# Kernel tuning notes

Hardware: AMD Instinct MI355X
Metric: run time of the kernel (lower is better)

Reference implementation:

```python
import jax, jax.numpy as jnp
import numpy as np

B, C, T, H, W = 4, 256, 16, 16, 16
C2 = C // 2  # 128


def setup_inputs() -> dict:
    key = jax.random.key(0)
    ks = jax.random.split(key, 12)
    s = 1.0 / np.sqrt(C)
    return {
        "X": jax.random.normal(ks[0], (B, C, T, H, W), dtype=jnp.float32),
        "pe": jax.random.uniform(ks[1], (C, T, H, W), dtype=jnp.float32),
        "task_q": jax.random.uniform(ks[2], (C2, T, H, W), dtype=jnp.float32),
        "task_k": jax.random.uniform(ks[3], (C2, T, H, W), dtype=jnp.float32),
        "task_v": jax.random.uniform(ks[4], (C2, T, H, W), dtype=jnp.float32),
        "Wq": jax.random.normal(ks[5], (C2, C), dtype=jnp.float32) * s,
        "bq": jnp.zeros((C2,), dtype=jnp.float32),
        "Wk": jax.random.normal(ks[6], (C2, C), dtype=jnp.float32) * s,
        "bk": jnp.zeros((C2,), dtype=jnp.float32),
        "Wv": jax.random.normal(ks[7], (C2, C), dtype=jnp.float32) * s,
        "bv": jnp.zeros((C2,), dtype=jnp.float32),
        "Wo": jax.random.normal(ks[8], (C, C2), dtype=jnp.float32) * s,
    }


def reference(X, pe, task_q, task_k, task_v, Wq, bq, Wk, bk, Wv, bv, Wo):
    b, c, t, h, w = X.shape
    c2 = Wq.shape[0]
    n = t * h * w
    Xp = X + pe  # broadcast [C,T,H,W] over batch

    def proj(Wm, bm, task):
        # 1x1x1 Conv3d == channel contraction; add bias and per-task offset
        y = jnp.einsum('bcthw,oc->bothw', Xp, Wm)
        return y + bm[:, None, None, None] + task  # [B,C2,T,H,W]

    q = proj(Wq, bq, task_q).reshape(b, c2, n).transpose(0, 2, 1)  # [B,N,C2]
    k = proj(Wk, bk, task_k).reshape(b, c2, n)                     # [B,C2,N]
    sim = jnp.matmul(q, k)                                         # [B,N,N]
    v = proj(Wv, bv, task_v).reshape(b, c2, n).transpose(0, 2, 1)  # [B,N,C2]
    # NOTE: original torch code computes softmax(sim) but then multiplies by
    # the RAW similarity matrix (softmax output is dead code). Faithful math:
    out = jnp.matmul(sim, v)                                       # [B,N,C2]
    # torch .reshape of contiguous [B,N,C2] -> [B,C2,T,H,W] (layout reinterpret)
    out = out.reshape(b, c2, t, h, w)
    out = jnp.einsum('bcthw,oc->bothw', out, Wo)  # out_conv, no bias
    return out + X
```

## Files before the change

kernel.cpp:

```cpp
#include <hip/hip_runtime.h>
#include <cstddef>

#define BB 4
#define CCH 256
#define C2 128
#define NN 4096
#define PM 384
#define KVS 32

typedef __attribute__((ext_vector_type(8))) short short8v;
typedef __attribute__((ext_vector_type(4))) short short4v;
typedef __attribute__((ext_vector_type(4))) float f32x4;

static __device__ __forceinline__ short f2bf(float f) {
    union { float f; unsigned u; } c; c.f = f;
    unsigned r = (c.u + 0x7FFFu + ((c.u >> 16) & 1u)) >> 16;
    return (short)r;
}

__global__ __launch_bounds__(256) void k_pack(
    const float* __restrict__ Wq, const float* __restrict__ bq,
    const float* __restrict__ Wk, const float* __restrict__ bk,
    const float* __restrict__ Wv, const float* __restrict__ bv,
    const float* __restrict__ Wo,
    short* __restrict__ wpackh, float* __restrict__ bpack,
    short* __restrict__ Woh)
{
    const int m = blockIdx.x;
    const int c = threadIdx.x;
    if (m < PM) {
        const float* w; const float* bs; int mm;
        if (m < C2)        { w = Wq; bs = bq; mm = m; }
        else if (m < 2*C2) { w = Wk; bs = bk; mm = m - C2; }
        else               { w = Wv; bs = bv; mm = m - 2*C2; }
        wpackh[m * CCH + c] = f2bf(w[mm * CCH + c]);
        if (c == 0) bpack[m] = bs[mm];
    } else {
        const int o = m - PM;
        if (c < C2) Woh[o * C2 + c] = f2bf(Wo[o * C2 + c]);
    }
}

__global__ __launch_bounds__(256) void k_xph(
    const float* __restrict__ X, const float* __restrict__ pe,
    short* __restrict__ XpH)
{
    const size_t e8 = ((size_t)blockIdx.x * 256 + threadIdx.x) * 8;
    const size_t r  = e8 & (size_t)(CCH * NN - 1);
    float4 x0 = *(const float4*)&X[e8];
    float4 x1 = *(const float4*)&X[e8 + 4];
    float4 p0 = *(const float4*)&pe[r];
    float4 p1 = *(const float4*)&pe[r + 4];
    short8v o;
    o[0] = f2bf(x0.x + p0.x); o[1] = f2bf(x0.y + p0.y);
    o[2] = f2bf(x0.z + p0.z); o[3] = f2bf(x0.w + p0.w);
    o[4] = f2bf(x1.x + p1.x); o[5] = f2bf(x1.y + p1.y);
    o[6] = f2bf(x1.z + p1.z); o[7] = f2bf(x1.w + p1.w);
    *(short8v*)&XpH[e8] = o;
}

#define LROW 40
#define TSP  136
__global__ __launch_bounds__(256) void k_projm(
    const short* __restrict__ XpH,
    const float* __restrict__ tq, const float* __restrict__ tk,
    const float* __restrict__ tv,
    const short* __restrict__ wpackh, const float* __restrict__ bpack,
    short* __restrict__ qt, short* __restrict__ kk, short* __restrict__ vv)
{
    __shared__ short smem[17408];
    short* As = smem;
    short* Bs = smem + 5120;
    const int b  = blockIdx.z;
    const int m0 = blockIdx.y * 128;
    const int n0 = blockIdx.x * 128;
    const int tid  = threadIdx.x;
    const int wave = tid >> 6;
    const int lane = tid & 63;
    const int lr = lane & 15, lg = lane >> 4;
    const int wm = wave >> 1, wn = wave & 1;
    const short* __restrict__ Xb = XpH + (size_t)b * CCH * NN;

    const int am  = tid >> 1;
    const int akb = tid & 1;
    const int cq  = tid >> 5;
    const int nq  = tid & 31;

    f32x4 acc[4][4];
#pragma unroll
    for (int i = 0; i < 4; ++i)
#pragma unroll
        for (int j = 0; j < 4; ++j) acc[i][j] = (f32x4){0.f, 0.f, 0.f, 0.f};

    for (int k0 = 0; k0 < CCH; k0 += 32) {
        {
            const size_t gsrc = (size_t)(m0 + am) * CCH + k0 + akb * 16;
            *(short8v*)&As[am * LROW + akb * 16]     = *(const short8v*)&wpackh[gsrc];
            *(short8v*)&As[am * LROW + akb * 16 + 8] = *(const short8v*)&wpackh[gsrc + 8];
        }
        short sreg[4][4];
#pragma unroll
        for (int j = 0; j < 4; ++j) {
            const int c = k0 + cq * 4 + j;
            short4v xv = *(const short4v*)&Xb[(size_t)c * NN + n0 + nq * 4];
            sreg[j][0] = xv.x; sreg[j][1] = xv.y; sreg[j][2] = xv.z; sreg[j][3] = xv.w;
        }
#pragma unroll
        for (int i = 0; i < 4; ++i) {
            short4v v; v.x = sreg[0][i]; v.y = sreg[1][i]; v.z = sreg[2][i]; v.w = sreg[3][i];
            *(short4v*)&Bs[(nq * 4 + i) * LROW + cq * 4] = v;
        }
        __syncthreads();
        short8v a[4], bfr[4];
#pragma unroll
        for (int fm = 0; fm < 4; ++fm)
            a[fm] = *(const short8v*)&As[(wm * 64 + fm * 16 + lr) * LROW + lg * 8];
#pragma unroll
        for (int fn = 0; fn < 4; ++fn)
            bfr[fn] = *(const short8v*)&Bs[(wn * 64 + fn * 16 + lr) * LROW + lg * 8];
#pragma unroll
        for (int fm = 0; fm < 4; ++fm)
#pragma unroll
            for (int fn = 0; fn < 4; ++fn)
                acc[fm][fn] = __builtin_amdgcn_mfma_f32_16x16x32_bf16(
                    a[fm], bfr[fn], acc[fm][fn], 0, 0, 0);
        __syncthreads();
    }

    short* Ts = smem;
    const int sel = m0 >> 7;
    if (sel == 0) {
#pragma unroll
        for (int fm = 0; fm < 4; ++fm)
#pragma unroll
            for (int fn = 0; fn < 4; ++fn) {
                const int n_l  = wn * 64 + fn * 16 + lr;
                const int m_lb = wm * 64 + fm * 16 + lg * 4;
                short4v v;
#pragma unroll
                for (int r = 0; r < 4; ++r) {
                    const int m_l = m_lb + r;
                    v[r] = f2bf(acc[fm][fn][r] + bpack[m_l]
                                + tq[(size_t)m_l * NN + n0 + n_l]);
                }
                *(short4v*)&Ts[n_l * TSP + m_lb] = v;
            }
        __syncthreads();
        const int n_l = tid >> 1, half = tid & 1;
        short* dst = qt + (size_t)b * NN * C2 + (size_t)(n0 + n_l) * C2 + half * 64;
        const short* src = &Ts[n_l * TSP + half * 64];
#pragma unroll
        for (int q2 = 0; q2 < 8; ++q2)
            *(short8v*)&dst[q2 * 8] = *(const short8v*)&src[q2 * 8];
    } else {
        const float* __restrict__ task = (sel == 1) ? tk : tv;
        short* kv = (sel == 1) ? kk : vv;
#pragma unroll
        for (int fm = 0; fm < 4; ++fm)
#pragma unroll
            for (int fn = 0; fn < 4; ++fn) {
                const int n_l = wn * 64 + fn * 16 + lr;
#pragma unroll
                for (int r = 0; r < 4; ++r) {
                    const int m_l = wm * 64 + fm * 16 + lg * 4 + r;
                    Ts[m_l * TSP + n_l] =
                        f2bf(acc[fm][fn][r] + bpack[m0 + m_l]
                             + task[(size_t)m_l * NN + n0 + n_l]);
                }
            }
        __syncthreads();
        const int m_l = tid >> 1, half = tid & 1;
        short* dst = kv + (size_t)b * C2 * NN + (size_t)m_l * NN + n0 + half * 64;
        const short* src = &Ts[m_l * TSP + half * 64];
#pragma unroll
        for (int q2 = 0; q2 < 8; ++q2)
            *(short8v*)&dst[q2 * 8] = *(const short8v*)&src[q2 * 8];
    }
}

__global__ __launch_bounds__(256) void k_kv(
    const short* __restrict__ kk, const short* __restrict__ vv,
    float* __restrict__ Mpart)
{
    const int b = blockIdx.y, s = blockIdx.x;
    const int tid = threadIdx.x;
    const int wave = tid >> 6, lane = tid & 63;
    const int lr = lane & 15, lg = lane >> 4;
    const int wi = wave >> 1, wj = wave & 1;
    const short* Kb = kk + (size_t)b * C2 * NN;
    const short* Vb = vv + (size_t)b * C2 * NN;
    const int nbase = s * 128;
    f32x4 acc[4][4];
#pragma unroll
    for (int i = 0; i < 4; ++i)
#pragma unroll
        for (int j = 0; j < 4; ++j) acc[i][j] = (f32x4){0.f, 0.f, 0.f, 0.f};

    for (int ks = 0; ks < 4; ++ks) {
        const int nn = nbase + ks * 32 + lg * 8;
        short8v a[4], bv8[4];
#pragma unroll
        for (int fi = 0; fi < 4; ++fi)
            a[fi] = *(const short8v*)&Kb[(size_t)(wi * 64 + fi * 16 + lr) * NN + nn];
#pragma unroll
        for (int fj = 0; fj < 4; ++fj)
            bv8[fj] = *(const short8v*)&Vb[(size_t)(wj * 64 + fj * 16 + lr) * NN + nn];
#pragma unroll
        for (int fi = 0; fi < 4; ++fi)
#pragma unroll
            for (int fj = 0; fj < 4; ++fj)
                acc[fi][fj] = __builtin_amdgcn_mfma_f32_16x16x32_bf16(
                    a[fi], bv8[fj], acc[fi][fj], 0, 0, 0);
    }
    float* Mp = Mpart + ((size_t)b * KVS + s) * C2 * C2;
#pragma unroll
    for (int fi = 0; fi < 4; ++fi)
#pragma unroll
        for (int fj = 0; fj < 4; ++fj) {
            const int j = wj * 64 + fj * 16 + lr;
#pragma unroll
            for (int r = 0; r < 4; ++r) {
                const int i = wi * 64 + fi * 16 + lg * 4 + r;
                Mp[(size_t)i * C2 + j] = acc[fi][fj][r];
            }
        }
}

__global__ __launch_bounds__(256) void k_kvred(
    const float* __restrict__ Mpart, short* __restrict__ Mt)
{
    const int b = blockIdx.y;
    const int i = blockIdx.x * 16 + (threadIdx.x >> 4);
    const int j0 = (threadIdx.x & 15) * 8;
    const float* p = Mpart + (size_t)b * KVS * C2 * C2 + (size_t)i * C2 + j0;
    float a8[8];
#pragma unroll
    for (int e = 0; e < 8; ++e) a8[e] = 0.f;
    for (int s = 0; s < KVS; ++s) {
        float4 v0 = *(const float4*)&p[(size_t)s * C2 * C2];
        float4 v1 = *(const float4*)&p[(size_t)s * C2 * C2 + 4];
        a8[0] += v0.x; a8[1] += v0.y; a8[2] += v0.z; a8[3] += v0.w;
        a8[4] += v1.x; a8[5] += v1.y; a8[6] += v1.z; a8[7] += v1.w;
    }
    short* mt = Mt + (size_t)b * C2 * C2;
#pragma unroll
    for (int e = 0; e < 8; ++e)
        mt[(size_t)(j0 + e) * C2 + i] = f2bf(a8[e]);
}

#define PSP 136
__global__ __launch_bounds__(256) void k_qmfinal(
    const short* __restrict__ qt, const short* __restrict__ Mt,
    const short* __restrict__ Woh,
    const float* __restrict__ X, float* __restrict__ out)
{
    __shared__ short Ps[64 * PSP];
    const int g  = blockIdx.x;
    const int jh = blockIdx.y;
    const int b  = blockIdx.z;
    const int tid = threadIdx.x;
    const int wave = tid >> 6, lane = tid & 63;
    const int lr = lane & 15, lg = lane >> 4;
    const short* Qb = qt + (size_t)b * NN * C2;
    const short* Mb = Mt + (size_t)b * C2 * C2;

    {
        const int wc = wave >> 1, wj = wave & 1;
        f32x4 acc1[4][2];
#pragma unroll
        for (int i = 0; i < 4; ++i)
#pragma unroll
            for (int j = 0; j < 2; ++j) acc1[i][j] = (f32x4){0.f, 0.f, 0.f, 0.f};
        for (int ks = 0; ks < 4; ++ks) {
            const int kb = ks * 32 + lg * 8;
            short8v a1[4], b1[2];
#pragma unroll
            for (int fc = 0; fc < 4; ++fc) {
                const int c = wc * 64 + fc * 16 + lr;
                a1[fc] = *(const short8v*)&Qb[(size_t)(c * 32 + g) * C2 + kb];
            }
#pragma unroll
            for (int fj = 0; fj < 2; ++fj) {
                const int j = jh * 64 + wj * 32 + fj * 16 + lr;
                b1[fj] = *(const short8v*)&Mb[(size_t)j * C2 + kb];
            }
#pragma unroll
            for (int fc = 0; fc < 4; ++fc)
#pragma unroll
                for (int fj = 0; fj < 2; ++fj)
                    acc1[fc][fj] = __builtin_amdgcn_mfma_f32_16x16x32_bf16(
                        a1[fc], b1[fj], acc1[fc][fj], 0, 0, 0);
        }
#pragma unroll
        for (int fc = 0; fc < 4; ++fc)
#pragma unroll
            for (int fj = 0; fj < 2; ++fj) {
                const int jp = wj * 32 + fj * 16 + lr;
                const int c0 = wc * 64 + fc * 16 + lg * 4;
                short4v v;
#pragma unroll
                for (int r = 0; r < 4; ++r) v[r] = f2bf(acc1[fc][fj][r]);
                *(short4v*)&Ps[jp * PSP + c0] = v;
            }
    }
    __syncthreads();

    {
        f32x4 acc2[4][4];
#pragma unroll
        for (int i = 0; i < 4; ++i)
#pragma unroll
            for (int j = 0; j < 4; ++j) acc2[i][j] = (f32x4){0.f, 0.f, 0.f, 0.f};
        for (int ks = 0; ks < 4; ++ks) {
            const int kb = ks * 32 + lg * 8;
            short8v a2[4], b2[4];
#pragma unroll
            for (int fo = 0; fo < 4; ++fo) {
                const int o = wave * 64 + fo * 16 + lr;
                a2[fo] = *(const short8v*)&Woh[(size_t)o * C2 + kb];
            }
#pragma unroll
            for (int fj = 0; fj < 4; ++fj)
                b2[fj] = *(const short8v*)&Ps[(fj * 16 + lr) * PSP + kb];
#pragma unroll
            for (int fo = 0; fo < 4; ++fo)
#pragma unroll
                for (int fj = 0; fj < 4; ++fj)
                    acc2[fo][fj] = __builtin_amdgcn_mfma_f32_16x16x32_bf16(
                        a2[fo], b2[fj], acc2[fo][fj], 0, 0, 0);
        }
        const float* Xb = X + (size_t)b * CCH * NN;
        float* Ob = out + (size_t)b * CCH * NN;
#pragma unroll
        for (int fo = 0; fo < 4; ++fo)
#pragma unroll
            for (int fj = 0; fj < 4; ++fj) {
                const int p = g * 128 + jh * 64 + fj * 16 + lr;
                const int ob = wave * 64 + fo * 16 + lg * 4;
#pragma unroll
                for (int r = 0; r < 4; ++r) {
                    const size_t ad = (size_t)(ob + r) * NN + p;
                    Ob[ad] = acc2[fo][fj][r] + Xb[ad];
                }
            }
    }
}

extern "C" void kernel_launch(void* const* d_in, const int* in_sizes, int n_in,
                              void* d_out, int out_size, void* d_ws, size_t ws_size,
                              hipStream_t stream) {
    const float* X  = (const float*)d_in[0];
    const float* pe = (const float*)d_in[1];
    const float* tq = (const float*)d_in[2];
    const float* tk = (const float*)d_in[3];
    const float* tv = (const float*)d_in[4];
    const float* Wq = (const float*)d_in[5];
    const float* bq = (const float*)d_in[6];
    const float* Wk = (const float*)d_in[7];
    const float* bk = (const float*)d_in[8];
    const float* Wv = (const float*)d_in[9];
    const float* bv = (const float*)d_in[10];
    const float* Wo = (const float*)d_in[11];
    float* out = (float*)d_out;

    float* ws     = (float*)d_ws;
    float* bpack  = ws;
    short* wpackh = (short*)(ws + 512);
    short* Woh    = (short*)(ws + 512 + 49152);
    short* qt     = (short*)(ws + 512 + 49152 + 16384);
    short* kk     = qt + (size_t)BB * NN * C2;
    short* vv     = kk + (size_t)BB * NN * C2;
    short* Mt     = vv + (size_t)BB * NN * C2;
    short* XpH    = Mt + (size_t)BB * C2 * C2;
    float* Mpart  = (float*)XpH;

    k_pack<<<dim3(PM + CCH), dim3(256), 0, stream>>>(
        Wq, bq, Wk, bk, Wv, bv, Wo, wpackh, bpack, Woh);
    k_xph<<<dim3((BB * CCH * NN) / (256 * 8)), dim3(256), 0, stream>>>(X, pe, XpH);
    k_projm<<<dim3(NN / 128, 3, BB), dim3(256), 0, stream>>>(
        XpH, tq, tk, tv, wpackh, bpack, qt, kk, vv);
    k_kv<<<dim3(KVS, BB), dim3(256), 0, stream>>>(kk, vv, Mpart);
    k_kvred<<<dim3(8, BB), dim3(256), 0, stream>>>(Mpart, Mt);
    k_qmfinal<<<dim3(32, 2, BB), dim3(256), 0, stream>>>(qt, Mt, Woh, X, out);
}
```

Before: 149.1 us.

## Merge prep kernels, fold KV reduction into final kernel, regroup q layout

```diff
diff --git a/kernel.cpp b/kernel.cpp
--- a/kernel.cpp
+++ b/kernel.cpp
@@ -6,7 +6,7 @@
 #define C2 128
 #define NN 4096
 #define PM 384
-#define KVS 32
+#define KVS 16
 
 typedef __attribute__((ext_vector_type(8))) short short8v;
 typedef __attribute__((ext_vector_type(4))) short short4v;
@@ -18,45 +18,44 @@
     return (short)r;
 }
 
-__global__ __launch_bounds__(256) void k_pack(
+__global__ __launch_bounds__(256) void k_prep(
+    const float* __restrict__ X, const float* __restrict__ pe,
     const float* __restrict__ Wq, const float* __restrict__ bq,
     const float* __restrict__ Wk, const float* __restrict__ bk,
     const float* __restrict__ Wv, const float* __restrict__ bv,
     const float* __restrict__ Wo,
-    short* __restrict__ wpackh, float* __restrict__ bpack,
-    short* __restrict__ Woh)
+    short* __restrict__ XpH, short* __restrict__ wpackh,
+    float* __restrict__ bpack, short* __restrict__ Woh)
 {
-    const int m = blockIdx.x;
-    const int c = threadIdx.x;
-    if (m < PM) {
-        const float* w; const float* bs; int mm;
-        if (m < C2)        { w = Wq; bs = bq; mm = m; }
-        else if (m < 2*C2) { w = Wk; bs = bk; mm = m - C2; }
-        else               { w = Wv; bs = bv; mm = m - 2*C2; }
-        wpackh[m * CCH + c] = f2bf(w[mm * CCH + c]);
-        if (c == 0) bpack[m] = bs[mm];
+    const int blk = blockIdx.x;
+    if (blk < 2048) {
+        const size_t e8 = ((size_t)blk * 256 + threadIdx.x) * 8;
+        const size_t r  = e8 & (size_t)(CCH * NN - 1);
+        float4 x0 = *(const float4*)&X[e8];
+        float4 x1 = *(const float4*)&X[e8 + 4];
+        float4 p0 = *(const float4*)&pe[r];
+        float4 p1 = *(const float4*)&pe[r + 4];
+        short8v o;
+        o[0] = f2bf(x0.x + p0.x); o[1] = f2bf(x0.y + p0.y);
+        o[2] = f2bf(x0.z + p0.z); o[3] = f2bf(x0.w + p0.w);
+        o[4] = f2bf(x1.x + p1.x); o[5] = f2bf(x1.y + p1.y);
+        o[6] = f2bf(x1.z + p1.z); o[7] = f2bf(x1.w + p1.w);
+        *(short8v*)&XpH[e8] = o;
     } else {
-        const int o = m - PM;
-        if (c < C2) Woh[o * C2 + c] = f2bf(Wo[o * C2 + c]);
-    }
-}
-
-__global__ __launch_bounds__(256) void k_xph(
-    const float* __restrict__ X, const float* __restrict__ pe,
-    short* __restrict__ XpH)
-{
-    const size_t e8 = ((size_t)blockIdx.x * 256 + threadIdx.x) * 8;
-    const size_t r  = e8 & (size_t)(CCH * NN - 1);
-    float4 x0 = *(const float4*)&X[e8];
-    float4 x1 = *(const float4*)&X[e8 + 4];
-    float4 p0 = *(const float4*)&pe[r];
-    float4 p1 = *(const float4*)&pe[r + 4];
-    short8v o;
-    o[0] = f2bf(x0.x + p0.x); o[1] = f2bf(x0.y + p0.y);
-    o[2] = f2bf(x0.z + p0.z); o[3] = f2bf(x0.w + p0.w);
-    o[4] = f2bf(x1.x + p1.x); o[5] = f2bf(x1.y + p1.y);
-    o[6] = f2bf(x1.z + p1.z); o[7] = f2bf(x1.w + p1.w);
-    *(short8v*)&XpH[e8] = o;
+        const int m = blk - 2048;
+        const int c = threadIdx.x;
+        if (m < PM) {
+            const float* w; const float* bs; int mm;
+            if (m < C2)        { w = Wq; bs = bq; mm = m; }
+            else if (m < 2*C2) { w = Wk; bs = bk; mm = m - C2; }
+            else               { w = Wv; bs = bv; mm = m - 2*C2; }
+            wpackh[m * CCH + c] = f2bf(w[mm * CCH + c]);
+            if (c == 0) bpack[m] = bs[mm];
+        } else {
+            const int o = m - PM;
+            if (c < C2) Woh[o * C2 + c] = f2bf(Wo[o * C2 + c]);
+        }
+    }
 }
 
 #define LROW 40
@@ -66,11 +65,10 @@
     const float* __restrict__ tq, const float* __restrict__ tk,
     const float* __restrict__ tv,
     const short* __restrict__ wpackh, const float* __restrict__ bpack,
-    short* __restrict__ qt, short* __restrict__ kk, short* __restrict__ vv)
+    short* __restrict__ qg, short* __restrict__ kk, short* __restrict__ vv)
 {
     __shared__ short smem[17408];
-    short* As = smem;
-    short* Bs = smem + 5120;
+    short* Bs = smem;
     const int b  = blockIdx.z;
     const int m0 = blockIdx.y * 128;
     const int n0 = blockIdx.x * 128;
@@ -81,10 +79,13 @@
     const int wm = wave >> 1, wn = wave & 1;
     const short* __restrict__ Xb = XpH + (size_t)b * CCH * NN;
 
-    const int am  = tid >> 1;
-    const int akb = tid & 1;
-    const int cq  = tid >> 5;
-    const int nq  = tid & 31;
+    const int cq = tid >> 5;
+    const int nq = tid & 31;
+
+    const short* Arow[4];
+#pragma unroll
+    for (int fm = 0; fm < 4; ++fm)
+        Arow[fm] = wpackh + (size_t)(m0 + wm * 64 + fm * 16 + lr) * CCH + lg * 8;
 
     f32x4 acc[4][4];
 #pragma unroll
@@ -92,12 +93,11 @@
 #pragma unroll
         for (int j = 0; j < 4; ++j) acc[i][j] = (f32x4){0.f, 0.f, 0.f, 0.f};
 
+    short8v a_cur[4], a_nxt[4];
+#pragma unroll
+    for (int fm = 0; fm < 4; ++fm) a_cur[fm] = *(const short8v*)&Arow[fm][0];
+
     for (int k0 = 0; k0 < CCH; k0 += 32) {
-        {
-            const size_t gsrc = (size_t)(m0 + am) * CCH + k0 + akb * 16;
-            *(short8v*)&As[am * LROW + akb * 16]     = *(const short8v*)&wpackh[gsrc];
-            *(short8v*)&As[am * LROW + akb * 16 + 8] = *(const short8v*)&wpackh[gsrc + 8];
-        }
         short sreg[4][4];
 #pragma unroll
         for (int j = 0; j < 4; ++j) {
@@ -111,10 +111,13 @@
             *(short4v*)&Bs[(nq * 4 + i) * LROW + cq * 4] = v;
         }
         __syncthreads();
-        short8v a[4], bfr[4];
-#pragma unroll
-        for (int fm = 0; fm < 4; ++fm)
-            a[fm] = *(const short8v*)&As[(wm * 64 + fm * 16 + lr) * LROW + lg * 8];
+        const bool more = (k0 + 32) < CCH;
+        if (more) {
+#pragma unroll
+            for (int fm = 0; fm < 4; ++fm)
+                a_nxt[fm] = *(const short8v*)&Arow[fm][k0 + 32];
+        }
+        short8v bfr[4];
 #pragma unroll
         for (int fn = 0; fn < 4; ++fn)
             bfr[fn] = *(const short8v*)&Bs[(wn * 64 + fn * 16 + lr) * LROW + lg * 8];
@@ -123,8 +126,12 @@
 #pragma unroll
             for (int fn = 0; fn < 4; ++fn)
                 acc[fm][fn] = __builtin_amdgcn_mfma_f32_16x16x32_bf16(
-                    a[fm], bfr[fn], acc[fm][fn], 0, 0, 0);
+                    a_cur[fm], bfr[fn], acc[fm][fn], 0, 0, 0);
         __syncthreads();
+        if (more) {
+#pragma unroll
+            for (int fm = 0; fm < 4; ++fm) a_cur[fm] = a_nxt[fm];
+        }
     }
 
     short* Ts = smem;
@@ -147,7 +154,9 @@
             }
         __syncthreads();
         const int n_l = tid >> 1, half = tid & 1;
-        short* dst = qt + (size_t)b * NN * C2 + (size_t)(n0 + n_l) * C2 + half * 64;
+        const int n = n0 + n_l;
+        short* dst = qg + (size_t)b * NN * C2
+                   + ((size_t)(n & 31) * 128 + (n >> 5)) * C2 + half * 64;
         const short* src = &Ts[n_l * TSP + half * 64];
 #pragma unroll
         for (int q2 = 0; q2 < 8; ++q2)
@@ -189,14 +198,14 @@
     const int wi = wave >> 1, wj = wave & 1;
     const short* Kb = kk + (size_t)b * C2 * NN;
     const short* Vb = vv + (size_t)b * C2 * NN;
-    const int nbase = s * 128;
+    const int nbase = s * 256;
     f32x4 acc[4][4];
 #pragma unroll
     for (int i = 0; i < 4; ++i)
 #pragma unroll
         for (int j = 0; j < 4; ++j) acc[i][j] = (f32x4){0.f, 0.f, 0.f, 0.f};
 
-    for (int ks = 0; ks < 4; ++ks) {
+    for (int ks = 0; ks < 8; ++ks) {
         const int nn = nbase + ks * 32 + lg * 8;
         short8v a[4], bv8[4];
 #pragma unroll
@@ -218,42 +227,19 @@
 #pragma unroll
         for (int fj = 0; fj < 4; ++fj) {
             const int j = wj * 64 + fj * 16 + lr;
-#pragma unroll
-            for (int r = 0; r < 4; ++r) {
-                const int i = wi * 64 + fi * 16 + lg * 4 + r;
-                Mp[(size_t)i * C2 + j] = acc[fi][fj][r];
-            }
-        }
-}
-
-__global__ __launch_bounds__(256) void k_kvred(
-    const float* __restrict__ Mpart, short* __restrict__ Mt)
-{
-    const int b = blockIdx.y;
-    const int i = blockIdx.x * 16 + (threadIdx.x >> 4);
-    const int j0 = (threadIdx.x & 15) * 8;
-    const float* p = Mpart + (size_t)b * KVS * C2 * C2 + (size_t)i * C2 + j0;
-    float a8[8];
-#pragma unroll
-    for (int e = 0; e < 8; ++e) a8[e] = 0.f;
-    for (int s = 0; s < KVS; ++s) {
-        float4 v0 = *(const float4*)&p[(size_t)s * C2 * C2];
-        float4 v1 = *(const float4*)&p[(size_t)s * C2 * C2 + 4];
-        a8[0] += v0.x; a8[1] += v0.y; a8[2] += v0.z; a8[3] += v0.w;
-        a8[4] += v1.x; a8[5] += v1.y; a8[6] += v1.z; a8[7] += v1.w;
-    }
-    short* mt = Mt + (size_t)b * C2 * C2;
-#pragma unroll
-    for (int e = 0; e < 8; ++e)
-        mt[(size_t)(j0 + e) * C2 + i] = f2bf(a8[e]);
-}
-
+            const int i = wi * 64 + fi * 16 + lg * 4;
+            *(float4*)&Mp[(size_t)j * C2 + i] = *(float4*)&acc[fi][fj];
+        }
+}
+
+#define MSP 136
 #define PSP 136
 __global__ __launch_bounds__(256) void k_qmfinal(
-    const short* __restrict__ qt, const short* __restrict__ Mt,
+    const short* __restrict__ qg, const float* __restrict__ Mpart,
     const short* __restrict__ Woh,
     const float* __restrict__ X, float* __restrict__ out)
 {
+    __shared__ short Ms[64 * MSP];
     __shared__ short Ps[64 * PSP];
     const int g  = blockIdx.x;
     const int jh = blockIdx.y;
@@ -261,11 +247,34 @@
     const int tid = threadIdx.x;
     const int wave = tid >> 6, lane = tid & 63;
     const int lr = lane & 15, lg = lane >> 4;
-    const short* Qb = qt + (size_t)b * NN * C2;
-    const short* Mb = Mt + (size_t)b * C2 * C2;
+
+    {
+        const int jloc = tid >> 2;
+        const int ib   = (tid & 3) * 4;
+        const float* base = Mpart + (size_t)b * KVS * C2 * C2
+                          + (size_t)(jh * 64 + jloc) * C2 + ib;
+#pragma unroll
+        for (int q = 0; q < 8; ++q) {
+            float4 s0 = {0.f, 0.f, 0.f, 0.f};
+            float4 s1 = {0.f, 0.f, 0.f, 0.f};
+#pragma unroll
+            for (int s = 0; s < KVS; s += 2) {
+                float4 v0 = *(const float4*)&base[(size_t)s * C2 * C2 + q * 16];
+                float4 v1 = *(const float4*)&base[(size_t)(s + 1) * C2 * C2 + q * 16];
+                s0.x += v0.x; s0.y += v0.y; s0.z += v0.z; s0.w += v0.w;
+                s1.x += v1.x; s1.y += v1.y; s1.z += v1.z; s1.w += v1.w;
+            }
+            short4v h;
+            h[0] = f2bf(s0.x + s1.x); h[1] = f2bf(s0.y + s1.y);
+            h[2] = f2bf(s0.z + s1.z); h[3] = f2bf(s0.w + s1.w);
+            *(short4v*)&Ms[jloc * MSP + ib + q * 16] = h;
+        }
+    }
+    __syncthreads();
 
     {
         const int wc = wave >> 1, wj = wave & 1;
+        const short* Qg = qg + (size_t)b * NN * C2 + (size_t)g * 128 * C2;
         f32x4 acc1[4][2];
 #pragma unroll
         for (int i = 0; i < 4; ++i)
@@ -275,15 +284,11 @@
             const int kb = ks * 32 + lg * 8;
             short8v a1[4], b1[2];
 #pragma unroll
-            for (int fc = 0; fc < 4; ++fc) {
-                const int c = wc * 64 + fc * 16 + lr;
-                a1[fc] = *(const short8v*)&Qb[(size_t)(c * 32 + g) * C2 + kb];
-            }
-#pragma unroll
-            for (int fj = 0; fj < 2; ++fj) {
-                const int j = jh * 64 + wj * 32 + fj * 16 + lr;
-                b1[fj] = *(const short8v*)&Mb[(size_t)j * C2 + kb];
-            }
+            for (int fc = 0; fc < 4; ++fc)
+                a1[fc] = *(const short8v*)&Qg[(size_t)(wc * 64 + fc * 16 + lr) * C2 + kb];
+#pragma unroll
+            for (int fj = 0; fj < 2; ++fj)
+                b1[fj] = *(const short8v*)&Ms[(wj * 32 + fj * 16 + lr) * MSP + kb];
 #pragma unroll
             for (int fc = 0; fc < 4; ++fc)
 #pragma unroll
@@ -315,10 +320,8 @@
             const int kb = ks * 32 + lg * 8;
             short8v a2[4], b2[4];
 #pragma unroll
-            for (int fo = 0; fo < 4; ++fo) {
-                const int o = wave * 64 + fo * 16 + lr;
-                a2[fo] = *(const short8v*)&Woh[(size_t)o * C2 + kb];
-            }
+            for (int fo = 0; fo < 4; ++fo)
+                a2[fo] = *(const short8v*)&Woh[(size_t)(wave * 64 + fo * 16 + lr) * C2 + kb];
 #pragma unroll
             for (int fj = 0; fj < 4; ++fj)
                 b2[fj] = *(const short8v*)&Ps[(fj * 16 + lr) * PSP + kb];
@@ -366,20 +369,17 @@
     float* ws     = (float*)d_ws;
     float* bpack  = ws;
     short* wpackh = (short*)(ws + 512);
-    short* Woh    = (short*)(ws + 512 + 49152);
-    short* qt     = (short*)(ws + 512 + 49152 + 16384);
-    short* kk     = qt + (size_t)BB * NN * C2;
+    short* Woh    = wpackh + (size_t)PM * CCH;
+    short* XpH    = Woh + (size_t)CCH * C2;
+    short* qg     = XpH + (size_t)BB * CCH * NN;
+    short* kk     = qg + (size_t)BB * NN * C2;
     short* vv     = kk + (size_t)BB * NN * C2;
-    short* Mt     = vv + (size_t)BB * NN * C2;
-    short* XpH    = Mt + (size_t)BB * C2 * C2;
-    float* Mpart  = (float*)XpH;
-
-    k_pack<<<dim3(PM + CCH), dim3(256), 0, stream>>>(
-        Wq, bq, Wk, bk, Wv, bv, Wo, wpackh, bpack, Woh);
-    k_xph<<<dim3((BB * CCH * NN) / (256 * 8)), dim3(256), 0, stream>>>(X, pe, XpH);
+    float* Mpart  = (float*)(vv + (size_t)BB * NN * C2);
+
+    k_prep<<<dim3(2048 + PM + CCH), dim3(256), 0, stream>>>(
+        X, pe, Wq, bq, Wk, bk, Wv, bv, Wo, XpH, wpackh, bpack, Woh);
     k_projm<<<dim3(NN / 128, 3, BB), dim3(256), 0, stream>>>(
-        XpH, tq, tk, tv, wpackh, bpack, qt, kk, vv);
+        XpH, tq, tk, tv, wpackh, bpack, qg, kk, vv);
     k_kv<<<dim3(KVS, BB), dim3(256), 0, stream>>>(kk, vv, Mpart);
-    k_kvred<<<dim3(8, BB), dim3(256), 0, stream>>>(Mpart, Mt);
-    k_qmfinal<<<dim3(32, 2, BB), dim3(256), 0, stream>>>(qt, Mt, Woh, X, out);
-}
+    k_qmfinal<<<dim3(32, 2, BB), dim3(256), 0, stream>>>(qg, Mpart, Woh, X, out);
+}
```

Result: slower. 158.6 us (+6.4%).
